# Performance work log

Hardware: AMD Instinct MI355X
Metric: run time of the kernel (lower is better)

The kernel has to match this reference:

```python
import jax, jax.numpy as jnp
import numpy as np

N_NODES = 50000
N_EDGES = 800000
HIDDEN = 128


def setup_inputs() -> dict:
    key = jax.random.key(0)
    ks = jax.random.split(key, 8)
    z = jax.random.normal(ks[0], (N_NODES, HIDDEN), dtype=jnp.float32)
    weights = jax.random.normal(ks[1], (N_EDGES, 1), dtype=jnp.float32)
    sources = jax.random.randint(ks[2], (N_EDGES,), 0, N_NODES)
    dests = jax.random.randint(ks[3], (N_EDGES,), 0, N_NODES)
    # Linear params (stored [in, out]); scale ~ 1/sqrt(fan_in) like torch default
    in_m = 2 * HIDDEN + 1
    in_u = 2 * HIDDEN
    Wm = jax.random.uniform(ks[4], (in_m, HIDDEN), dtype=jnp.float32, minval=-1.0, maxval=1.0) / np.sqrt(in_m)
    bm = jax.random.uniform(ks[5], (HIDDEN,), dtype=jnp.float32, minval=-1.0, maxval=1.0) / np.sqrt(in_m)
    Wu = jax.random.uniform(ks[6], (in_u, HIDDEN), dtype=jnp.float32, minval=-1.0, maxval=1.0) / np.sqrt(in_u)
    bu = jax.random.uniform(ks[7], (HIDDEN,), dtype=jnp.float32, minval=-1.0, maxval=1.0) / np.sqrt(in_u)
    return {"z": z, "weights": weights, "sources": sources, "dests": dests,
            "Wm": Wm, "bm": bm, "Wu": Wu, "bu": bu}


def reference(z, weights, sources, dests, Wm, bm, Wu, bu):
    n = z.shape[0]
    # gather + concat message input: [E, 2d+1]
    inp = jnp.concatenate([z[dests], z[sources], weights], axis=1)
    messages = inp @ Wm + bm                      # [E, d]
    # scatter_reduce amax over destination nodes; empty segments -> -inf
    m = jax.ops.segment_max(messages, dests, num_segments=n)
    m = jnp.where(jnp.isneginf(m), jnp.zeros_like(m), m)
    h = jnp.concatenate([z, m], axis=1) @ Wu + bu  # [N, d]
    return h
```

## Files before the change

kernel.cpp:

```cpp
#include <hip/hip_runtime.h>
#include <math.h>

#define HIDDEN 128
#define PAD_DEG 64
#define NPART 8
#define CHUNK 4096
#define CNT_STRIDE 16
#define NSCATTER_BLOCKS 256
#define XCC_GETREG_IMM 63508

typedef __attribute__((ext_vector_type(8))) _Float16 f16x8;
typedef __attribute__((ext_vector_type(4))) float f32x4;
typedef __attribute__((ext_vector_type(2))) _Float16 h2;

__device__ inline unsigned short f2h(float x) {
    _Float16 h = (_Float16)x;
    return __builtin_bit_cast(unsigned short, h);
}
__device__ inline float h2f(unsigned short u) {
    return (float)__builtin_bit_cast(_Float16, u);
}
__device__ inline float h2f_lo(unsigned int u) { return h2f((unsigned short)(u & 0xffff)); }
__device__ inline float h2f_hi(unsigned int u) { return h2f((unsigned short)(u >> 16)); }
__device__ inline h2 hmax2(h2 a, h2 b) {
    h2 r;
    r[0] = a[0] > b[0] ? a[0] : b[0];
    r[1] = a[1] > b[1] ? a[1] : b[1];
    return r;
}

__global__ void prep_kernel(const float* __restrict__ Wm, const float* __restrict__ Wu,
                            unsigned short* __restrict__ WmT0, unsigned short* __restrict__ WmT1,
                            unsigned short* __restrict__ WuT, float* __restrict__ wlast,
                            int* __restrict__ counts, int* __restrict__ tick, int n) {
    int t = blockIdx.x * blockDim.x + threadIdx.x;
    if (t < 16384) {
        int nn = t >> 7, k = t & 127;
        WmT0[t] = f2h(Wm[k * 128 + nn]);
    } else if (t < 32768) {
        int s = t - 16384;
        int nn = s >> 7, k = s & 127;
        WmT1[s] = f2h(Wm[(128 + k) * 128 + nn]);
    } else if (t < 65536) {
        int s = t - 32768;
        int nn = s >> 8, k = s & 255;
        WuT[s] = f2h(Wu[k * 128 + nn]);
    } else if (t < 65664) {
        int i = t - 65536;
        wlast[i] = Wm[256 * 128 + i];
    } else if (t < 65664 + 4 * n) {
        ((int4*)counts)[t - 65664] = make_int4(0, 0, 0, 0);
    } else if (t < 65664 + 4 * n + 128) {
        tick[t - 65664 - 4 * n] = 0;
    }
}

__global__ __launch_bounds__(256) void fused_sg(const int* __restrict__ dests,
                                                const int* __restrict__ sources,
                                                const float* __restrict__ weights,
                                                int* __restrict__ counts,
                                                int* __restrict__ tick,
                                                unsigned int* __restrict__ edge_pk,
                                                int E, int span, int n, int nchunks,
                                                const float* __restrict__ Z,
                                                const unsigned short* __restrict__ WmT0,
                                                const unsigned short* __restrict__ WmT1,
                                                unsigned short* __restrict__ P1h,
                                                unsigned short* __restrict__ P2h,
                                                int nscatter) {
    __shared__ unsigned short As[64][136];
    __shared__ unsigned short Bs[64][136];
    __shared__ int s_chunk;

    if (blockIdx.x < nscatter) {
        const int xcd = (int)(__builtin_amdgcn_s_getreg(XCC_GETREG_IMM) & 7);
        const int lo = xcd * span;
        const int hi = min(lo + span, n);

        for (int it = 0; it <= nchunks; ++it) {
            if (threadIdx.x == 0) {
                s_chunk = __hip_atomic_fetch_add(&tick[xcd * 16], 1,
                                                 __ATOMIC_RELAXED, __HIP_MEMORY_SCOPE_AGENT);
            }
            __syncthreads();
            const int chunk = s_chunk;
            __syncthreads();
            if (chunk >= nchunks || chunk < 0) break;

            const int base = chunk * CHUNK + threadIdx.x * 4;
            int dd[16];
            unsigned int pk[16];
            int pos[16];

#pragma unroll
            for (int g = 0; g < 4; ++g) {
                int e = base + g * 1024;
                if (e + 3 < E) {
                    int4 dq = *(const int4*)&dests[e];
                    int4 sq = *(const int4*)&sources[e];
                    float4 wq = *(const float4*)&weights[e];
                    dd[g * 4 + 0] = dq.x; dd[g * 4 + 1] = dq.y;
                    dd[g * 4 + 2] = dq.z; dd[g * 4 + 3] = dq.w;
                    pk[g * 4 + 0] = (unsigned int)(sq.x & 0xffff) | ((unsigned int)f2h(wq.x) << 16);
                    pk[g * 4 + 1] = (unsigned int)(sq.y & 0xffff) | ((unsigned int)f2h(wq.y) << 16);
                    pk[g * 4 + 2] = (unsigned int)(sq.z & 0xffff) | ((unsigned int)f2h(wq.z) << 16);
                    pk[g * 4 + 3] = (unsigned int)(sq.w & 0xffff) | ((unsigned int)f2h(wq.w) << 16);
                } else {
#pragma unroll
                    for (int j = 0; j < 4; ++j) {
                        int ej = e + j;
                        if (ej < E) {
                            dd[g * 4 + j] = dests[ej];
                            pk[g * 4 + j] = (unsigned int)(sources[ej] & 0xffff) |
                                            ((unsigned int)f2h(weights[ej]) << 16);
                        } else {
                            dd[g * 4 + j] = -1;
                            pk[g * 4 + j] = 0;
                        }
                    }
                }
            }

#pragma unroll
            for (int k = 0; k < 16; ++k) {
                bool act = (dd[k] >= lo) && (dd[k] < hi);
                pos[k] = act ? atomicAdd(&counts[(size_t)dd[k] * CNT_STRIDE], 1) : PAD_DEG;
            }

#pragma unroll
            for (int k = 0; k < 16; ++k) {
                if (pos[k] < PAD_DEG) {
                    edge_pk[(size_t)dd[k] * PAD_DEG + pos[k]] = pk[k];
                }
            }
        }
        return;
    }

    const int m0 = (blockIdx.x - nscatter) * 64;
    const int tid = threadIdx.x;
    const int wave = tid >> 6, lane = tid & 63;
    const int l15 = lane & 15, q = lane >> 4;
    const int wrow = wave * 16;

#pragma unroll
    for (int i = 0; i < 4; ++i) {
        int f = tid + i * 256;
        int row = f >> 4, c8 = f & 15;
        int gr = min(m0 + row, n - 1);
        const float4* src = (const float4*)&Z[(size_t)gr * 128 + c8 * 8];
        float4 a = src[0], b = src[1];
        f16x8 hv;
        hv[0] = (_Float16)a.x; hv[1] = (_Float16)a.y; hv[2] = (_Float16)a.z; hv[3] = (_Float16)a.w;
        hv[4] = (_Float16)b.x; hv[5] = (_Float16)b.y; hv[6] = (_Float16)b.z; hv[7] = (_Float16)b.w;
        *(f16x8*)&As[row][c8 * 8] = hv;
    }

    for (int part = 0; part < 2; ++part) {
        const float4* bsrc = (const float4*)(part == 0 ? WmT0 : WmT1);
        unsigned short* Out = part == 0 ? P1h : P2h;

        for (int nh = 0; nh < 2; ++nh) {
#pragma unroll
            for (int i = 0; i < 4; ++i) {
                int f = tid + i * 256;
                int row = f >> 4, c4 = f & 15;
                *(float4*)&Bs[row][c4 * 8] = bsrc[(nh * 64 + row) * 16 + c4];
            }
            __syncthreads();

            f32x4 acc[4];
#pragma unroll
            for (int nt = 0; nt < 4; ++nt) acc[nt] = (f32x4){0.f, 0.f, 0.f, 0.f};

#pragma unroll
            for (int ks = 0; ks < 4; ++ks) {
                int k0 = ks * 32;
                f16x8 a = *(const f16x8*)&As[wrow + l15][k0 + q * 8];
#pragma unroll
                for (int nt = 0; nt < 4; ++nt) {
                    f16x8 b = *(const f16x8*)&Bs[nt * 16 + l15][k0 + q * 8];
                    acc[nt] = __builtin_amdgcn_mfma_f32_16x16x32_f16(a, b, acc[nt], 0, 0, 0);
                }
            }

#pragma unroll
            for (int nt = 0; nt < 4; ++nt) {
#pragma unroll
                for (int r = 0; r < 4; ++r) {
                    int row = m0 + wrow + q * 4 + r;
                    if (row < n) Out[(size_t)row * 128 + nh * 64 + nt * 16 + l15] = f2h(acc[nt][r]);
                }
            }
            __syncthreads();
        }
    }
}

__device__ inline void ladder(const uint4* __restrict__ P2q, int pk, int cnt, int j,
                              int l16, int e4, h2 wl0, h2 wl1, h2 wl2, h2 wl3,
                              h2& a0, h2& a1, h2& a2, h2& a3) {
    for (; j + 16 <= cnt; j += 16) {
        unsigned int pa = (unsigned int)__shfl(pk, j + e4);
        unsigned int pb = (unsigned int)__shfl(pk, j + 4 + e4);
        unsigned int pc = (unsigned int)__shfl(pk, j + 8 + e4);
        unsigned int pd = (unsigned int)__shfl(pk, j + 12 + e4);
        uint4 ua = P2q[(size_t)(pa & 0xffff) * 16 + l16];
        uint4 ub = P2q[(size_t)(pb & 0xffff) * 16 + l16];
        uint4 uc = P2q[(size_t)(pc & 0xffff) * 16 + l16];
        uint4 ud = P2q[(size_t)(pd & 0xffff) * 16 + l16];
        h2 wva = __builtin_bit_cast(h2, (pa & 0xffff0000u) | (pa >> 16));
        h2 wvb = __builtin_bit_cast(h2, (pb & 0xffff0000u) | (pb >> 16));
        h2 wvc = __builtin_bit_cast(h2, (pc & 0xffff0000u) | (pc >> 16));
        h2 wvd = __builtin_bit_cast(h2, (pd & 0xffff0000u) | (pd >> 16));
        a0 = hmax2(a0, wva * wl0 + __builtin_bit_cast(h2, ua.x));
        a1 = hmax2(a1, wva * wl1 + __builtin_bit_cast(h2, ua.y));
        a2 = hmax2(a2, wva * wl2 + __builtin_bit_cast(h2, ua.z));
        a3 = hmax2(a3, wva * wl3 + __builtin_bit_cast(h2, ua.w));
        a0 = hmax2(a0, wvb * wl0 + __builtin_bit_cast(h2, ub.x));
        a1 = hmax2(a1, wvb * wl1 + __builtin_bit_cast(h2, ub.y));
        a2 = hmax2(a2, wvb * wl2 + __builtin_bit_cast(h2, ub.z));
        a3 = hmax2(a3, wvb * wl3 + __builtin_bit_cast(h2, ub.w));
        a0 = hmax2(a0, wvc * wl0 + __builtin_bit_cast(h2, uc.x));
        a1 = hmax2(a1, wvc * wl1 + __builtin_bit_cast(h2, uc.y));
        a2 = hmax2(a2, wvc * wl2 + __builtin_bit_cast(h2, uc.z));
        a3 = hmax2(a3, wvc * wl3 + __builtin_bit_cast(h2, uc.w));
        a0 = hmax2(a0, wvd * wl0 + __builtin_bit_cast(h2, ud.x));
        a1 = hmax2(a1, wvd * wl1 + __builtin_bit_cast(h2, ud.y));
        a2 = hmax2(a2, wvd * wl2 + __builtin_bit_cast(h2, ud.z));
        a3 = hmax2(a3, wvd * wl3 + __builtin_bit_cast(h2, ud.w));
    }
    for (; j + 8 <= cnt; j += 8) {
        unsigned int pa = (unsigned int)__shfl(pk, j + e4);
        unsigned int pb = (unsigned int)__shfl(pk, j + 4 + e4);
        uint4 ua = P2q[(size_t)(pa & 0xffff) * 16 + l16];
        uint4 ub = P2q[(size_t)(pb & 0xffff) * 16 + l16];
        h2 wva = __builtin_bit_cast(h2, (pa & 0xffff0000u) | (pa >> 16));
        h2 wvb = __builtin_bit_cast(h2, (pb & 0xffff0000u) | (pb >> 16));
        a0 = hmax2(a0, wva * wl0 + __builtin_bit_cast(h2, ua.x));
        a1 = hmax2(a1, wva * wl1 + __builtin_bit_cast(h2, ua.y));
        a2 = hmax2(a2, wva * wl2 + __builtin_bit_cast(h2, ua.z));
        a3 = hmax2(a3, wva * wl3 + __builtin_bit_cast(h2, ua.w));
        a0 = hmax2(a0, wvb * wl0 + __builtin_bit_cast(h2, ub.x));
        a1 = hmax2(a1, wvb * wl1 + __builtin_bit_cast(h2, ub.y));
        a2 = hmax2(a2, wvb * wl2 + __builtin_bit_cast(h2, ub.z));
        a3 = hmax2(a3, wvb * wl3 + __builtin_bit_cast(h2, ub.w));
    }
    for (; j < cnt; j += 4) {
        int idx = j + e4;
        bool valid = idx < cnt;
        unsigned int pa = (unsigned int)__shfl(pk, valid ? idx : 0);
        if (valid) {
            uint4 ua = P2q[(size_t)(pa & 0xffff) * 16 + l16];
            h2 wva = __builtin_bit_cast(h2, (pa & 0xffff0000u) | (pa >> 16));
            a0 = hmax2(a0, wva * wl0 + __builtin_bit_cast(h2, ua.x));
            a1 = hmax2(a1, wva * wl1 + __builtin_bit_cast(h2, ua.y));
            a2 = hmax2(a2, wva * wl2 + __builtin_bit_cast(h2, ua.z));
            a3 = hmax2(a3, wva * wl3 + __builtin_bit_cast(h2, ua.w));
        }
    }
}

__global__ __launch_bounds__(256) void segmax_kernel(const unsigned short* __restrict__ P1h,
                                                     const unsigned short* __restrict__ P2h,
                                                     const int* __restrict__ counts,
                                                     const unsigned int* __restrict__ edge_pk,
                                                     const float* __restrict__ wlast,
                                                     const float* __restrict__ bm,
                                                     unsigned short* __restrict__ Mh, int n) {
    const int wave = threadIdx.x >> 6;
    const int lane = threadIdx.x & 63;
    const int va = blockIdx.x * 8 + wave * 2;
    const int vb = va + 1;
    if (va >= n) return;

    const int l16 = lane & 15;
    const int e4 = lane >> 4;
    const uint4* P2q = (const uint4*)P2h;
    const int cntA = min(counts[(size_t)va * CNT_STRIDE], PAD_DEG);
    const int cntB = (vb < n) ? min(counts[(size_t)vb * CNT_STRIDE], PAD_DEG) : 0;

    int pkA = (lane < cntA) ? (int)edge_pk[(size_t)va * PAD_DEG + lane] : 0;
    int pkB = (lane < cntB) ? (int)edge_pk[(size_t)vb * PAD_DEG + lane] : 0;

    float4 wfa = ((const float4*)wlast)[l16 * 2];
    float4 wfb = ((const float4*)wlast)[l16 * 2 + 1];
    h2 wl0, wl1, wl2, wl3;
    wl0[0] = (_Float16)wfa.x; wl0[1] = (_Float16)wfa.y;
    wl1[0] = (_Float16)wfa.z; wl1[1] = (_Float16)wfa.w;
    wl2[0] = (_Float16)wfb.x; wl2[1] = (_Float16)wfb.y;
    wl3[0] = (_Float16)wfb.z; wl3[1] = (_Float16)wfb.w;

    const h2 NEGINF = __builtin_bit_cast(h2, 0xFC00FC00u);
    h2 aA0 = NEGINF, aA1 = NEGINF, aA2 = NEGINF, aA3 = NEGINF;
    h2 aB0 = NEGINF, aB1 = NEGINF, aB2 = NEGINF, aB3 = NEGINF;

    int j = 0;
    for (; j + 8 <= cntA && j + 8 <= cntB; j += 8) {
        unsigned int pa = (unsigned int)__shfl(pkA, j + e4);
        unsigned int pb = (unsigned int)__shfl(pkA, j + 4 + e4);
        unsigned int pc = (unsigned int)__shfl(pkB, j + e4);
        unsigned int pd = (unsigned int)__shfl(pkB, j + 4 + e4);
        uint4 ua = P2q[(size_t)(pa & 0xffff) * 16 + l16];
        uint4 ub = P2q[(size_t)(pb & 0xffff) * 16 + l16];
        uint4 uc = P2q[(size_t)(pc & 0xffff) * 16 + l16];
        uint4 ud = P2q[(size_t)(pd & 0xffff) * 16 + l16];
        h2 wva = __builtin_bit_cast(h2, (pa & 0xffff0000u) | (pa >> 16));
        h2 wvb = __builtin_bit_cast(h2, (pb & 0xffff0000u) | (pb >> 16));
        h2 wvc = __builtin_bit_cast(h2, (pc & 0xffff0000u) | (pc >> 16));
        h2 wvd = __builtin_bit_cast(h2, (pd & 0xffff0000u) | (pd >> 16));
        aA0 = hmax2(aA0, wva * wl0 + __builtin_bit_cast(h2, ua.x));
        aA1 = hmax2(aA1, wva * wl1 + __builtin_bit_cast(h2, ua.y));
        aA2 = hmax2(aA2, wva * wl2 + __builtin_bit_cast(h2, ua.z));
        aA3 = hmax2(aA3, wva * wl3 + __builtin_bit_cast(h2, ua.w));
        aA0 = hmax2(aA0, wvb * wl0 + __builtin_bit_cast(h2, ub.x));
        aA1 = hmax2(aA1, wvb * wl1 + __builtin_bit_cast(h2, ub.y));
        aA2 = hmax2(aA2, wvb * wl2 + __builtin_bit_cast(h2, ub.z));
        aA3 = hmax2(aA3, wvb * wl3 + __builtin_bit_cast(h2, ub.w));
        aB0 = hmax2(aB0, wvc * wl0 + __builtin_bit_cast(h2, uc.x));
        aB1 = hmax2(aB1, wvc * wl1 + __builtin_bit_cast(h2, uc.y));
        aB2 = hmax2(aB2, wvc * wl2 + __builtin_bit_cast(h2, uc.z));
        aB3 = hmax2(aB3, wvc * wl3 + __builtin_bit_cast(h2, uc.w));
        aB0 = hmax2(aB0, wvd * wl0 + __builtin_bit_cast(h2, ud.x));
        aB1 = hmax2(aB1, wvd * wl1 + __builtin_bit_cast(h2, ud.y));
        aB2 = hmax2(aB2, wvd * wl2 + __builtin_bit_cast(h2, ud.z));
        aB3 = hmax2(aB3, wvd * wl3 + __builtin_bit_cast(h2, ud.w));
    }
    ladder(P2q, pkA, cntA, j, l16, e4, wl0, wl1, wl2, wl3, aA0, aA1, aA2, aA3);
    ladder(P2q, pkB, cntB, j, l16, e4, wl0, wl1, wl2, wl3, aB0, aB1, aB2, aB3);

    aA0 = hmax2(aA0, __builtin_bit_cast(h2, __shfl_xor(__builtin_bit_cast(int, aA0), 16)));
    aA1 = hmax2(aA1, __builtin_bit_cast(h2, __shfl_xor(__builtin_bit_cast(int, aA1), 16)));
    aA2 = hmax2(aA2, __builtin_bit_cast(h2, __shfl_xor(__builtin_bit_cast(int, aA2), 16)));
    aA3 = hmax2(aA3, __builtin_bit_cast(h2, __shfl_xor(__builtin_bit_cast(int, aA3), 16)));
    aA0 = hmax2(aA0, __builtin_bit_cast(h2, __shfl_xor(__builtin_bit_cast(int, aA0), 32)));
    aA1 = hmax2(aA1, __builtin_bit_cast(h2, __shfl_xor(__builtin_bit_cast(int, aA1), 32)));
    aA2 = hmax2(aA2, __builtin_bit_cast(h2, __shfl_xor(__builtin_bit_cast(int, aA2), 32)));
    aA3 = hmax2(aA3, __builtin_bit_cast(h2, __shfl_xor(__builtin_bit_cast(int, aA3), 32)));
    aB0 = hmax2(aB0, __builtin_bit_cast(h2, __shfl_xor(__builtin_bit_cast(int, aB0), 16)));
    aB1 = hmax2(aB1, __builtin_bit_cast(h2, __shfl_xor(__builtin_bit_cast(int, aB1), 16)));
    aB2 = hmax2(aB2, __builtin_bit_cast(h2, __shfl_xor(__builtin_bit_cast(int, aB2), 16)));
    aB3 = hmax2(aB3, __builtin_bit_cast(h2, __shfl_xor(__builtin_bit_cast(int, aB3), 16)));
    aB0 = hmax2(aB0, __builtin_bit_cast(h2, __shfl_xor(__builtin_bit_cast(int, aB0), 32)));
    aB1 = hmax2(aB1, __builtin_bit_cast(h2, __shfl_xor(__builtin_bit_cast(int, aB1), 32)));
    aB2 = hmax2(aB2, __builtin_bit_cast(h2, __shfl_xor(__builtin_bit_cast(int, aB2), 32)));
    aB3 = hmax2(aB3, __builtin_bit_cast(h2, __shfl_xor(__builtin_bit_cast(int, aB3), 32)));

    if (e4 == 0) {
        float4 b0 = ((const float4*)bm)[l16 * 2];
        float4 b1 = ((const float4*)bm)[l16 * 2 + 1];
        unsigned int zh = (unsigned int)f2h(0.f);
        unsigned int zz = zh | (zh << 16);

        {
            uint4 o = make_uint4(zz, zz, zz, zz);
            if (cntA > 0) {
                uint4 p1 = ((const uint4*)P1h)[(size_t)va * 16 + l16];
                float m0 = h2f_lo(p1.x) + b0.x + (float)aA0[0];
                float m1 = h2f_hi(p1.x) + b0.y + (float)aA0[1];
                float m2 = h2f_lo(p1.y) + b0.z + (float)aA1[0];
                float m3 = h2f_hi(p1.y) + b0.w + (float)aA1[1];
                float m4 = h2f_lo(p1.z) + b1.x + (float)aA2[0];
                float m5 = h2f_hi(p1.z) + b1.y + (float)aA2[1];
                float m6 = h2f_lo(p1.w) + b1.z + (float)aA3[0];
                float m7 = h2f_hi(p1.w) + b1.w + (float)aA3[1];
                o.x = (unsigned int)f2h(m0) | ((unsigned int)f2h(m1) << 16);
                o.y = (unsigned int)f2h(m2) | ((unsigned int)f2h(m3) << 16);
                o.z = (unsigned int)f2h(m4) | ((unsigned int)f2h(m5) << 16);
                o.w = (unsigned int)f2h(m6) | ((unsigned int)f2h(m7) << 16);
            }
            ((uint4*)Mh)[(size_t)va * 16 + l16] = o;
        }
        if (vb < n) {
            uint4 o = make_uint4(zz, zz, zz, zz);
            if (cntB > 0) {
                uint4 p1 = ((const uint4*)P1h)[(size_t)vb * 16 + l16];
                float m0 = h2f_lo(p1.x) + b0.x + (float)aB0[0];
                float m1 = h2f_hi(p1.x) + b0.y + (float)aB0[1];
                float m2 = h2f_lo(p1.y) + b0.z + (float)aB1[0];
                float m3 = h2f_hi(p1.y) + b0.w + (float)aB1[1];
                float m4 = h2f_lo(p1.z) + b1.x + (float)aB2[0];
                float m5 = h2f_hi(p1.z) + b1.y + (float)aB2[1];
                float m6 = h2f_lo(p1.w) + b1.z + (float)aB3[0];
                float m7 = h2f_hi(p1.w) + b1.w + (float)aB3[1];
                o.x = (unsigned int)f2h(m0) | ((unsigned int)f2h(m1) << 16);
                o.y = (unsigned int)f2h(m2) | ((unsigned int)f2h(m3) << 16);
                o.z = (unsigned int)f2h(m4) | ((unsigned int)f2h(m5) << 16);
                o.w = (unsigned int)f2h(m6) | ((unsigned int)f2h(m7) << 16);
            }
            ((uint4*)Mh)[(size_t)vb * 16 + l16] = o;
        }
    }
}

__global__ __launch_bounds__(256) void gemm_out(const float* __restrict__ Z,
                                                const unsigned short* __restrict__ Mh,
                                                const unsigned short* __restrict__ WuT,
                                                const float* __restrict__ bu,
                                                float* __restrict__ H, int n) {
    __shared__ unsigned short As[64][136];
    __shared__ unsigned short Bs[64][136];

    const int m0 = blockIdx.x * 64;
    const int tid = threadIdx.x;
    const int wave = tid >> 6, lane = tid & 63;
    const int l15 = lane & 15, q = lane >> 4;
    const int wrow = wave * 16;

    f32x4 acc[8];
#pragma unroll
    for (int i = 0; i < 8; ++i) acc[i] = (f32x4){0.f, 0.f, 0.f, 0.f};

    for (int h = 0; h < 2; ++h) {
        if (h == 0) {
#pragma unroll
            for (int i = 0; i < 4; ++i) {
                int f = tid + i * 256;
                int row = f >> 4, c8 = f & 15;
                int gr = min(m0 + row, n - 1);
                const float4* src = (const float4*)&Z[(size_t)gr * 128 + c8 * 8];
                float4 a = src[0], b = src[1];
                f16x8 hv;
                hv[0] = (_Float16)a.x; hv[1] = (_Float16)a.y; hv[2] = (_Float16)a.z; hv[3] = (_Float16)a.w;
                hv[4] = (_Float16)b.x; hv[5] = (_Float16)b.y; hv[6] = (_Float16)b.z; hv[7] = (_Float16)b.w;
                *(f16x8*)&As[row][c8 * 8] = hv;
            }
        } else {
#pragma unroll
            for (int i = 0; i < 4; ++i) {
                int f = tid + i * 256;
                int row = f >> 4, c4 = f & 15;
                int gr = min(m0 + row, n - 1);
                *(float4*)&As[row][c4 * 8] = ((const float4*)&Mh[(size_t)gr * 128])[c4];
            }
        }

        for (int nh = 0; nh < 2; ++nh) {
#pragma unroll
            for (int i = 0; i < 4; ++i) {
                int f = tid + i * 256;
                int row = f >> 4, c4 = f & 15;
                *(float4*)&Bs[row][c4 * 8] = ((const float4*)WuT)[(nh * 64 + row) * 32 + h * 16 + c4];
            }
            __syncthreads();

#pragma unroll
            for (int ks = 0; ks < 4; ++ks) {
                int k0 = ks * 32;
                f16x8 a = *(const f16x8*)&As[wrow + l15][k0 + q * 8];
#pragma unroll
                for (int nt = 0; nt < 4; ++nt) {
                    f16x8 b = *(const f16x8*)&Bs[nt * 16 + l15][k0 + q * 8];
                    acc[nh * 4 + nt] = __builtin_amdgcn_mfma_f32_16x16x32_f16(a, b, acc[nh * 4 + nt], 0, 0, 0);
                }
            }
            __syncthreads();
        }
    }

#pragma unroll
    for (int nh = 0; nh < 2; ++nh) {
#pragma unroll
        for (int nt = 0; nt < 4; ++nt) {
            int col = nh * 64 + nt * 16 + l15;
            float bias = bu[col];
#pragma unroll
            for (int r = 0; r < 4; ++r) {
                int row = m0 + wrow + q * 4 + r;
                if (row < n) H[(size_t)row * 128 + col] = acc[nh * 4 + nt][r] + bias;
            }
        }
    }
}

extern "C" void kernel_launch(void* const* d_in, const int* in_sizes, int n_in,
                              void* d_out, int out_size, void* d_ws, size_t ws_size,
                              hipStream_t stream) {
    const float* z = (const float*)d_in[0];
    const float* weights = (const float*)d_in[1];
    const int* sources = (const int*)d_in[2];
    const int* dests = (const int*)d_in[3];
    const float* Wm = (const float*)d_in[4];
    const float* bm = (const float*)d_in[5];
    const float* Wu = (const float*)d_in[6];
    const float* bu = (const float*)d_in[7];

    const int n = in_sizes[0] / HIDDEN;
    const int E = in_sizes[1];
    float* H = (float*)d_out;

    char* w = (char*)d_ws;
    auto alloc = [&](size_t bytes) { void* p = w; w += (bytes + 255) & ~(size_t)255; return p; };
    unsigned short* P1h = (unsigned short*)alloc((size_t)n * 128 * 2);
    unsigned short* Mh  = (unsigned short*)alloc((size_t)n * 128 * 2);
    unsigned short* WmT0 = (unsigned short*)alloc(16384 * 2);
    unsigned short* WmT1 = (unsigned short*)alloc(16384 * 2);
    unsigned short* WuT  = (unsigned short*)alloc(32768 * 2);
    float* wlast = (float*)alloc(128 * 4);
    int* counts  = (int*)alloc((size_t)n * CNT_STRIDE * 4);
    int* tick    = (int*)alloc(128 * 4);
    unsigned int* edge_pk = (unsigned int*)alloc((size_t)n * PAD_DEG * 4);

    unsigned short* P2h = (unsigned short*)d_out;

    const int mblocks = (n + 63) / 64;
    const int prep_threads = 65664 + 4 * n + 128;
    const int span = (n + NPART - 1) / NPART;
    const int nchunks = (E + CHUNK - 1) / CHUNK;
    const int nscatter = NSCATTER_BLOCKS;

    prep_kernel<<<(prep_threads + 255) / 256, 256, 0, stream>>>(Wm, Wu, WmT0, WmT1, WuT,
                                                                wlast, counts, tick, n);
    fused_sg<<<nscatter + mblocks, 256, 0, stream>>>(dests, sources, weights, counts, tick,
                                                     edge_pk, E, span, n, nchunks,
                                                     z, WmT0, WmT1, P1h, P2h, nscatter);
    segmax_kernel<<<(n + 7) / 8, 256, 0, stream>>>(P1h, P2h, counts, edge_pk,
                                                   wlast, bm, Mh, n);
    gemm_out<<<mblocks, 256, 0, stream>>>(z, Mh, WuT, bu, H, n);
}
```

Before: 180.8 us.

## Split output GEMM and overlap Z-half with segment-max gather kernel

The output projection is split into a Z·Wu_top part and an M·Wu_bottom part. The Z part runs as extra blocks in the same launch as the segment-max kernel, so the dense GEMM can overlap the gather-bound aggregation. A separate kernel then adds M·Wu_bottom into H with a read-modify-write. M is written in place over the P1h buffer, and P2h moves from the output buffer into workspace so H can be written early. In exchange, H is read and written a second time, and the segmax blocks now share the GPU with GEMM blocks.

```diff
diff --git a/kernel.cpp b/kernel.cpp
--- a/kernel.cpp
+++ b/kernel.cpp
@@ -261,143 +261,208 @@
     }
 }
 
-__global__ __launch_bounds__(256) void segmax_kernel(const unsigned short* __restrict__ P1h,
-                                                     const unsigned short* __restrict__ P2h,
-                                                     const int* __restrict__ counts,
-                                                     const unsigned int* __restrict__ edge_pk,
-                                                     const float* __restrict__ wlast,
-                                                     const float* __restrict__ bm,
-                                                     unsigned short* __restrict__ Mh, int n) {
-    const int wave = threadIdx.x >> 6;
-    const int lane = threadIdx.x & 63;
-    const int va = blockIdx.x * 8 + wave * 2;
-    const int vb = va + 1;
-    if (va >= n) return;
-
-    const int l16 = lane & 15;
-    const int e4 = lane >> 4;
-    const uint4* P2q = (const uint4*)P2h;
-    const int cntA = min(counts[(size_t)va * CNT_STRIDE], PAD_DEG);
-    const int cntB = (vb < n) ? min(counts[(size_t)vb * CNT_STRIDE], PAD_DEG) : 0;
-
-    int pkA = (lane < cntA) ? (int)edge_pk[(size_t)va * PAD_DEG + lane] : 0;
-    int pkB = (lane < cntB) ? (int)edge_pk[(size_t)vb * PAD_DEG + lane] : 0;
-
-    float4 wfa = ((const float4*)wlast)[l16 * 2];
-    float4 wfb = ((const float4*)wlast)[l16 * 2 + 1];
-    h2 wl0, wl1, wl2, wl3;
-    wl0[0] = (_Float16)wfa.x; wl0[1] = (_Float16)wfa.y;
-    wl1[0] = (_Float16)wfa.z; wl1[1] = (_Float16)wfa.w;
-    wl2[0] = (_Float16)wfb.x; wl2[1] = (_Float16)wfb.y;
-    wl3[0] = (_Float16)wfb.z; wl3[1] = (_Float16)wfb.w;
-
-    const h2 NEGINF = __builtin_bit_cast(h2, 0xFC00FC00u);
-    h2 aA0 = NEGINF, aA1 = NEGINF, aA2 = NEGINF, aA3 = NEGINF;
-    h2 aB0 = NEGINF, aB1 = NEGINF, aB2 = NEGINF, aB3 = NEGINF;
-
-    int j = 0;
-    for (; j + 8 <= cntA && j + 8 <= cntB; j += 8) {
-        unsigned int pa = (unsigned int)__shfl(pkA, j + e4);
-        unsigned int pb = (unsigned int)__shfl(pkA, j + 4 + e4);
-        unsigned int pc = (unsigned int)__shfl(pkB, j + e4);
-        unsigned int pd = (unsigned int)__shfl(pkB, j + 4 + e4);
-        uint4 ua = P2q[(size_t)(pa & 0xffff) * 16 + l16];
-        uint4 ub = P2q[(size_t)(pb & 0xffff) * 16 + l16];
-        uint4 uc = P2q[(size_t)(pc & 0xffff) * 16 + l16];
-        uint4 ud = P2q[(size_t)(pd & 0xffff) * 16 + l16];
-        h2 wva = __builtin_bit_cast(h2, (pa & 0xffff0000u) | (pa >> 16));
-        h2 wvb = __builtin_bit_cast(h2, (pb & 0xffff0000u) | (pb >> 16));
-        h2 wvc = __builtin_bit_cast(h2, (pc & 0xffff0000u) | (pc >> 16));
-        h2 wvd = __builtin_bit_cast(h2, (pd & 0xffff0000u) | (pd >> 16));
-        aA0 = hmax2(aA0, wva * wl0 + __builtin_bit_cast(h2, ua.x));
-        aA1 = hmax2(aA1, wva * wl1 + __builtin_bit_cast(h2, ua.y));
-        aA2 = hmax2(aA2, wva * wl2 + __builtin_bit_cast(h2, ua.z));
-        aA3 = hmax2(aA3, wva * wl3 + __builtin_bit_cast(h2, ua.w));
-        aA0 = hmax2(aA0, wvb * wl0 + __builtin_bit_cast(h2, ub.x));
-        aA1 = hmax2(aA1, wvb * wl1 + __builtin_bit_cast(h2, ub.y));
-        aA2 = hmax2(aA2, wvb * wl2 + __builtin_bit_cast(h2, ub.z));
-        aA3 = hmax2(aA3, wvb * wl3 + __builtin_bit_cast(h2, ub.w));
-        aB0 = hmax2(aB0, wvc * wl0 + __builtin_bit_cast(h2, uc.x));
-        aB1 = hmax2(aB1, wvc * wl1 + __builtin_bit_cast(h2, uc.y));
-        aB2 = hmax2(aB2, wvc * wl2 + __builtin_bit_cast(h2, uc.z));
-        aB3 = hmax2(aB3, wvc * wl3 + __builtin_bit_cast(h2, uc.w));
-        aB0 = hmax2(aB0, wvd * wl0 + __builtin_bit_cast(h2, ud.x));
-        aB1 = hmax2(aB1, wvd * wl1 + __builtin_bit_cast(h2, ud.y));
-        aB2 = hmax2(aB2, wvd * wl2 + __builtin_bit_cast(h2, ud.z));
-        aB3 = hmax2(aB3, wvd * wl3 + __builtin_bit_cast(h2, ud.w));
-    }
-    ladder(P2q, pkA, cntA, j, l16, e4, wl0, wl1, wl2, wl3, aA0, aA1, aA2, aA3);
-    ladder(P2q, pkB, cntB, j, l16, e4, wl0, wl1, wl2, wl3, aB0, aB1, aB2, aB3);
-
-    aA0 = hmax2(aA0, __builtin_bit_cast(h2, __shfl_xor(__builtin_bit_cast(int, aA0), 16)));
-    aA1 = hmax2(aA1, __builtin_bit_cast(h2, __shfl_xor(__builtin_bit_cast(int, aA1), 16)));
-    aA2 = hmax2(aA2, __builtin_bit_cast(h2, __shfl_xor(__builtin_bit_cast(int, aA2), 16)));
-    aA3 = hmax2(aA3, __builtin_bit_cast(h2, __shfl_xor(__builtin_bit_cast(int, aA3), 16)));
-    aA0 = hmax2(aA0, __builtin_bit_cast(h2, __shfl_xor(__builtin_bit_cast(int, aA0), 32)));
-    aA1 = hmax2(aA1, __builtin_bit_cast(h2, __shfl_xor(__builtin_bit_cast(int, aA1), 32)));
-    aA2 = hmax2(aA2, __builtin_bit_cast(h2, __shfl_xor(__builtin_bit_cast(int, aA2), 32)));
-    aA3 = hmax2(aA3, __builtin_bit_cast(h2, __shfl_xor(__builtin_bit_cast(int, aA3), 32)));
-    aB0 = hmax2(aB0, __builtin_bit_cast(h2, __shfl_xor(__builtin_bit_cast(int, aB0), 16)));
-    aB1 = hmax2(aB1, __builtin_bit_cast(h2, __shfl_xor(__builtin_bit_cast(int, aB1), 16)));
-    aB2 = hmax2(aB2, __builtin_bit_cast(h2, __shfl_xor(__builtin_bit_cast(int, aB2), 16)));
-    aB3 = hmax2(aB3, __builtin_bit_cast(h2, __shfl_xor(__builtin_bit_cast(int, aB3), 16)));
-    aB0 = hmax2(aB0, __builtin_bit_cast(h2, __shfl_xor(__builtin_bit_cast(int, aB0), 32)));
-    aB1 = hmax2(aB1, __builtin_bit_cast(h2, __shfl_xor(__builtin_bit_cast(int, aB1), 32)));
-    aB2 = hmax2(aB2, __builtin_bit_cast(h2, __shfl_xor(__builtin_bit_cast(int, aB2), 32)));
-    aB3 = hmax2(aB3, __builtin_bit_cast(h2, __shfl_xor(__builtin_bit_cast(int, aB3), 32)));
-
-    if (e4 == 0) {
-        float4 b0 = ((const float4*)bm)[l16 * 2];
-        float4 b1 = ((const float4*)bm)[l16 * 2 + 1];
-        unsigned int zh = (unsigned int)f2h(0.f);
-        unsigned int zz = zh | (zh << 16);
-
-        {
-            uint4 o = make_uint4(zz, zz, zz, zz);
-            if (cntA > 0) {
-                uint4 p1 = ((const uint4*)P1h)[(size_t)va * 16 + l16];
-                float m0 = h2f_lo(p1.x) + b0.x + (float)aA0[0];
-                float m1 = h2f_hi(p1.x) + b0.y + (float)aA0[1];
-                float m2 = h2f_lo(p1.y) + b0.z + (float)aA1[0];
-                float m3 = h2f_hi(p1.y) + b0.w + (float)aA1[1];
-                float m4 = h2f_lo(p1.z) + b1.x + (float)aA2[0];
-                float m5 = h2f_hi(p1.z) + b1.y + (float)aA2[1];
-                float m6 = h2f_lo(p1.w) + b1.z + (float)aA3[0];
-                float m7 = h2f_hi(p1.w) + b1.w + (float)aA3[1];
-                o.x = (unsigned int)f2h(m0) | ((unsigned int)f2h(m1) << 16);
-                o.y = (unsigned int)f2h(m2) | ((unsigned int)f2h(m3) << 16);
-                o.z = (unsigned int)f2h(m4) | ((unsigned int)f2h(m5) << 16);
-                o.w = (unsigned int)f2h(m6) | ((unsigned int)f2h(m7) << 16);
-            }
-            ((uint4*)Mh)[(size_t)va * 16 + l16] = o;
-        }
-        if (vb < n) {
-            uint4 o = make_uint4(zz, zz, zz, zz);
-            if (cntB > 0) {
-                uint4 p1 = ((const uint4*)P1h)[(size_t)vb * 16 + l16];
-                float m0 = h2f_lo(p1.x) + b0.x + (float)aB0[0];
-                float m1 = h2f_hi(p1.x) + b0.y + (float)aB0[1];
-                float m2 = h2f_lo(p1.y) + b0.z + (float)aB1[0];
-                float m3 = h2f_hi(p1.y) + b0.w + (float)aB1[1];
-                float m4 = h2f_lo(p1.z) + b1.x + (float)aB2[0];
-                float m5 = h2f_hi(p1.z) + b1.y + (float)aB2[1];
-                float m6 = h2f_lo(p1.w) + b1.z + (float)aB3[0];
-                float m7 = h2f_hi(p1.w) + b1.w + (float)aB3[1];
-                o.x = (unsigned int)f2h(m0) | ((unsigned int)f2h(m1) << 16);
-                o.y = (unsigned int)f2h(m2) | ((unsigned int)f2h(m3) << 16);
-                o.z = (unsigned int)f2h(m4) | ((unsigned int)f2h(m5) << 16);
-                o.w = (unsigned int)f2h(m6) | ((unsigned int)f2h(m7) << 16);
-            }
-            ((uint4*)Mh)[(size_t)vb * 16 + l16] = o;
-        }
-    }
-}
-
-__global__ __launch_bounds__(256) void gemm_out(const float* __restrict__ Z,
-                                                const unsigned short* __restrict__ Mh,
-                                                const unsigned short* __restrict__ WuT,
-                                                const float* __restrict__ bu,
-                                                float* __restrict__ H, int n) {
+__global__ __launch_bounds__(256) void seg_gz(const unsigned short* P1h,
+                                              const unsigned short* __restrict__ P2h,
+                                              const int* __restrict__ counts,
+                                              const unsigned int* __restrict__ edge_pk,
+                                              const float* __restrict__ wlast,
+                                              const float* __restrict__ bm,
+                                              unsigned short* Mh,
+                                              const float* __restrict__ Z,
+                                              const unsigned short* __restrict__ WuT,
+                                              const float* __restrict__ bu,
+                                              float* __restrict__ H,
+                                              int n, int nseg) {
+    __shared__ unsigned short As[64][136];
+    __shared__ unsigned short Bs[64][136];
+
+    if (blockIdx.x < nseg) {
+        const int wave = threadIdx.x >> 6;
+        const int lane = threadIdx.x & 63;
+        const int va = blockIdx.x * 8 + wave * 2;
+        const int vb = va + 1;
+        if (va >= n) return;
+
+        const int l16 = lane & 15;
+        const int e4 = lane >> 4;
+        const uint4* P2q = (const uint4*)P2h;
+        const int cntA = min(counts[(size_t)va * CNT_STRIDE], PAD_DEG);
+        const int cntB = (vb < n) ? min(counts[(size_t)vb * CNT_STRIDE], PAD_DEG) : 0;
+
+        int pkA = (lane < cntA) ? (int)edge_pk[(size_t)va * PAD_DEG + lane] : 0;
+        int pkB = (lane < cntB) ? (int)edge_pk[(size_t)vb * PAD_DEG + lane] : 0;
+
+        float4 wfa = ((const float4*)wlast)[l16 * 2];
+        float4 wfb = ((const float4*)wlast)[l16 * 2 + 1];
+        h2 wl0, wl1, wl2, wl3;
+        wl0[0] = (_Float16)wfa.x; wl0[1] = (_Float16)wfa.y;
+        wl1[0] = (_Float16)wfa.z; wl1[1] = (_Float16)wfa.w;
+        wl2[0] = (_Float16)wfb.x; wl2[1] = (_Float16)wfb.y;
+        wl3[0] = (_Float16)wfb.z; wl3[1] = (_Float16)wfb.w;
+
+        const h2 NEGINF = __builtin_bit_cast(h2, 0xFC00FC00u);
+        h2 aA0 = NEGINF, aA1 = NEGINF, aA2 = NEGINF, aA3 = NEGINF;
+        h2 aB0 = NEGINF, aB1 = NEGINF, aB2 = NEGINF, aB3 = NEGINF;
+
+        int j = 0;
+        for (; j + 8 <= cntA && j + 8 <= cntB; j += 8) {
+            unsigned int pa = (unsigned int)__shfl(pkA, j + e4);
+            unsigned int pb = (unsigned int)__shfl(pkA, j + 4 + e4);
+            unsigned int pc = (unsigned int)__shfl(pkB, j + e4);
+            unsigned int pd = (unsigned int)__shfl(pkB, j + 4 + e4);
+            uint4 ua = P2q[(size_t)(pa & 0xffff) * 16 + l16];
+            uint4 ub = P2q[(size_t)(pb & 0xffff) * 16 + l16];
+            uint4 uc = P2q[(size_t)(pc & 0xffff) * 16 + l16];
+            uint4 ud = P2q[(size_t)(pd & 0xffff) * 16 + l16];
+            h2 wva = __builtin_bit_cast(h2, (pa & 0xffff0000u) | (pa >> 16));
+            h2 wvb = __builtin_bit_cast(h2, (pb & 0xffff0000u) | (pb >> 16));
+            h2 wvc = __builtin_bit_cast(h2, (pc & 0xffff0000u) | (pc >> 16));
+            h2 wvd = __builtin_bit_cast(h2, (pd & 0xffff0000u) | (pd >> 16));
+            aA0 = hmax2(aA0, wva * wl0 + __builtin_bit_cast(h2, ua.x));
+            aA1 = hmax2(aA1, wva * wl1 + __builtin_bit_cast(h2, ua.y));
+            aA2 = hmax2(aA2, wva * wl2 + __builtin_bit_cast(h2, ua.z));
+            aA3 = hmax2(aA3, wva * wl3 + __builtin_bit_cast(h2, ua.w));
+            aA0 = hmax2(aA0, wvb * wl0 + __builtin_bit_cast(h2, ub.x));
+            aA1 = hmax2(aA1, wvb * wl1 + __builtin_bit_cast(h2, ub.y));
+            aA2 = hmax2(aA2, wvb * wl2 + __builtin_bit_cast(h2, ub.z));
+            aA3 = hmax2(aA3, wvb * wl3 + __builtin_bit_cast(h2, ub.w));
+            aB0 = hmax2(aB0, wvc * wl0 + __builtin_bit_cast(h2, uc.x));
+            aB1 = hmax2(aB1, wvc * wl1 + __builtin_bit_cast(h2, uc.y));
+            aB2 = hmax2(aB2, wvc * wl2 + __builtin_bit_cast(h2, uc.z));
+            aB3 = hmax2(aB3, wvc * wl3 + __builtin_bit_cast(h2, uc.w));
+            aB0 = hmax2(aB0, wvd * wl0 + __builtin_bit_cast(h2, ud.x));
+            aB1 = hmax2(aB1, wvd * wl1 + __builtin_bit_cast(h2, ud.y));
+            aB2 = hmax2(aB2, wvd * wl2 + __builtin_bit_cast(h2, ud.z));
+            aB3 = hmax2(aB3, wvd * wl3 + __builtin_bit_cast(h2, ud.w));
+        }
+        ladder(P2q, pkA, cntA, j, l16, e4, wl0, wl1, wl2, wl3, aA0, aA1, aA2, aA3);
+        ladder(P2q, pkB, cntB, j, l16, e4, wl0, wl1, wl2, wl3, aB0, aB1, aB2, aB3);
+
+        aA0 = hmax2(aA0, __builtin_bit_cast(h2, __shfl_xor(__builtin_bit_cast(int, aA0), 16)));
+        aA1 = hmax2(aA1, __builtin_bit_cast(h2, __shfl_xor(__builtin_bit_cast(int, aA1), 16)));
+        aA2 = hmax2(aA2, __builtin_bit_cast(h2, __shfl_xor(__builtin_bit_cast(int, aA2), 16)));
+        aA3 = hmax2(aA3, __builtin_bit_cast(h2, __shfl_xor(__builtin_bit_cast(int, aA3), 16)));
+        aA0 = hmax2(aA0, __builtin_bit_cast(h2, __shfl_xor(__builtin_bit_cast(int, aA0), 32)));
+        aA1 = hmax2(aA1, __builtin_bit_cast(h2, __shfl_xor(__builtin_bit_cast(int, aA1), 32)));
+        aA2 = hmax2(aA2, __builtin_bit_cast(h2, __shfl_xor(__builtin_bit_cast(int, aA2), 32)));
+        aA3 = hmax2(aA3, __builtin_bit_cast(h2, __shfl_xor(__builtin_bit_cast(int, aA3), 32)));
+        aB0 = hmax2(aB0, __builtin_bit_cast(h2, __shfl_xor(__builtin_bit_cast(int, aB0), 16)));
+        aB1 = hmax2(aB1, __builtin_bit_cast(h2, __shfl_xor(__builtin_bit_cast(int, aB1), 16)));
+        aB2 = hmax2(aB2, __builtin_bit_cast(h2, __shfl_xor(__builtin_bit_cast(int, aB2), 16)));
+        aB3 = hmax2(aB3, __builtin_bit_cast(h2, __shfl_xor(__builtin_bit_cast(int, aB3), 16)));
+        aB0 = hmax2(aB0, __builtin_bit_cast(h2, __shfl_xor(__builtin_bit_cast(int, aB0), 32)));
+        aB1 = hmax2(aB1, __builtin_bit_cast(h2, __shfl_xor(__builtin_bit_cast(int, aB1), 32)));
+        aB2 = hmax2(aB2, __builtin_bit_cast(h2, __shfl_xor(__builtin_bit_cast(int, aB2), 32)));
+        aB3 = hmax2(aB3, __builtin_bit_cast(h2, __shfl_xor(__builtin_bit_cast(int, aB3), 32)));
+
+        if (e4 == 0) {
+            float4 b0 = ((const float4*)bm)[l16 * 2];
+            float4 b1 = ((const float4*)bm)[l16 * 2 + 1];
+            unsigned int zh = (unsigned int)f2h(0.f);
+            unsigned int zz = zh | (zh << 16);
+
+            {
+                uint4 o = make_uint4(zz, zz, zz, zz);
+                if (cntA > 0) {
+                    uint4 p1 = ((const uint4*)P1h)[(size_t)va * 16 + l16];
+                    float m0 = h2f_lo(p1.x) + b0.x + (float)aA0[0];
+                    float m1 = h2f_hi(p1.x) + b0.y + (float)aA0[1];
+                    float m2 = h2f_lo(p1.y) + b0.z + (float)aA1[0];
+                    float m3 = h2f_hi(p1.y) + b0.w + (float)aA1[1];
+                    float m4 = h2f_lo(p1.z) + b1.x + (float)aA2[0];
+                    float m5 = h2f_hi(p1.z) + b1.y + (float)aA2[1];
+                    float m6 = h2f_lo(p1.w) + b1.z + (float)aA3[0];
+                    float m7 = h2f_hi(p1.w) + b1.w + (float)aA3[1];
+                    o.x = (unsigned int)f2h(m0) | ((unsigned int)f2h(m1) << 16);
+                    o.y = (unsigned int)f2h(m2) | ((unsigned int)f2h(m3) << 16);
+                    o.z = (unsigned int)f2h(m4) | ((unsigned int)f2h(m5) << 16);
+                    o.w = (unsigned int)f2h(m6) | ((unsigned int)f2h(m7) << 16);
+                }
+                ((uint4*)Mh)[(size_t)va * 16 + l16] = o;
+            }
+            if (vb < n) {
+                uint4 o = make_uint4(zz, zz, zz, zz);
+                if (cntB > 0) {
+                    uint4 p1 = ((const uint4*)P1h)[(size_t)vb * 16 + l16];
+                    float m0 = h2f_lo(p1.x) + b0.x + (float)aB0[0];
+                    float m1 = h2f_hi(p1.x) + b0.y + (float)aB0[1];
+                    float m2 = h2f_lo(p1.y) + b0.z + (float)aB1[0];
+                    float m3 = h2f_hi(p1.y) + b0.w + (float)aB1[1];
+                    float m4 = h2f_lo(p1.z) + b1.x + (float)aB2[0];
+                    float m5 = h2f_hi(p1.z) + b1.y + (float)aB2[1];
+                    float m6 = h2f_lo(p1.w) + b1.z + (float)aB3[0];
+                    float m7 = h2f_hi(p1.w) + b1.w + (float)aB3[1];
+                    o.x = (unsigned int)f2h(m0) | ((unsigned int)f2h(m1) << 16);
+                    o.y = (unsigned int)f2h(m2) | ((unsigned int)f2h(m3) << 16);
+                    o.z = (unsigned int)f2h(m4) | ((unsigned int)f2h(m5) << 16);
+                    o.w = (unsigned int)f2h(m6) | ((unsigned int)f2h(m7) << 16);
+                }
+                ((uint4*)Mh)[(size_t)vb * 16 + l16] = o;
+            }
+        }
+        return;
+    }
+
+    const int m0 = (blockIdx.x - nseg) * 64;
+    const int tid = threadIdx.x;
+    const int wave = tid >> 6, lane = tid & 63;
+    const int l15 = lane & 15, q = lane >> 4;
+    const int wrow = wave * 16;
+
+#pragma unroll
+    for (int i = 0; i < 4; ++i) {
+        int f = tid + i * 256;
+        int row = f >> 4, c8 = f & 15;
+        int gr = min(m0 + row, n - 1);
+        const float4* src = (const float4*)&Z[(size_t)gr * 128 + c8 * 8];
+        float4 a = src[0], b = src[1];
+        f16x8 hv;
+        hv[0] = (_Float16)a.x; hv[1] = (_Float16)a.y; hv[2] = (_Float16)a.z; hv[3] = (_Float16)a.w;
+        hv[4] = (_Float16)b.x; hv[5] = (_Float16)b.y; hv[6] = (_Float16)b.z; hv[7] = (_Float16)b.w;
+        *(f16x8*)&As[row][c8 * 8] = hv;
+    }
+
+    for (int nh = 0; nh < 2; ++nh) {
+#pragma unroll
+        for (int i = 0; i < 4; ++i) {
+            int f = tid + i * 256;
+            int row = f >> 4, c4 = f & 15;
+            *(float4*)&Bs[row][c4 * 8] = ((const float4*)WuT)[(nh * 64 + row) * 32 + c4];
+        }
+        __syncthreads();
+
+        f32x4 acc[4];
+#pragma unroll
+        for (int nt = 0; nt < 4; ++nt) acc[nt] = (f32x4){0.f, 0.f, 0.f, 0.f};
+
+#pragma unroll
+        for (int ks = 0; ks < 4; ++ks) {
+            int k0 = ks * 32;
+            f16x8 a = *(const f16x8*)&As[wrow + l15][k0 + q * 8];
+#pragma unroll
+            for (int nt = 0; nt < 4; ++nt) {
+                f16x8 b = *(const f16x8*)&Bs[nt * 16 + l15][k0 + q * 8];
+                acc[nt] = __builtin_amdgcn_mfma_f32_16x16x32_f16(a, b, acc[nt], 0, 0, 0);
+            }
+        }
+
+#pragma unroll
+        for (int nt = 0; nt < 4; ++nt) {
+            int col = nh * 64 + nt * 16 + l15;
+            float bias = bu[col];
+#pragma unroll
+            for (int r = 0; r < 4; ++r) {
+                int row = m0 + wrow + q * 4 + r;
+                if (row < n) H[(size_t)row * 128 + col] = acc[nt][r] + bias;
+            }
+        }
+        __syncthreads();
+    }
+}
+
+__global__ __launch_bounds__(256) void gemm_m(const unsigned short* __restrict__ Mh,
+                                              const unsigned short* __restrict__ WuT,
+                                              float* __restrict__ H, int n) {
     __shared__ unsigned short As[64][136];
     __shared__ unsigned short Bs[64][136];
 
@@ -407,69 +472,48 @@
     const int l15 = lane & 15, q = lane >> 4;
     const int wrow = wave * 16;
 
-    f32x4 acc[8];
-#pragma unroll
-    for (int i = 0; i < 8; ++i) acc[i] = (f32x4){0.f, 0.f, 0.f, 0.f};
-
-    for (int h = 0; h < 2; ++h) {
-        if (h == 0) {
-#pragma unroll
-            for (int i = 0; i < 4; ++i) {
-                int f = tid + i * 256;
-                int row = f >> 4, c8 = f & 15;
-                int gr = min(m0 + row, n - 1);
-                const float4* src = (const float4*)&Z[(size_t)gr * 128 + c8 * 8];
-                float4 a = src[0], b = src[1];
-                f16x8 hv;
-                hv[0] = (_Float16)a.x; hv[1] = (_Float16)a.y; hv[2] = (_Float16)a.z; hv[3] = (_Float16)a.w;
-                hv[4] = (_Float16)b.x; hv[5] = (_Float16)b.y; hv[6] = (_Float16)b.z; hv[7] = (_Float16)b.w;
-                *(f16x8*)&As[row][c8 * 8] = hv;
-            }
-        } else {
-#pragma unroll
-            for (int i = 0; i < 4; ++i) {
-                int f = tid + i * 256;
-                int row = f >> 4, c4 = f & 15;
-                int gr = min(m0 + row, n - 1);
-                *(float4*)&As[row][c4 * 8] = ((const float4*)&Mh[(size_t)gr * 128])[c4];
-            }
-        }
-
-        for (int nh = 0; nh < 2; ++nh) {
-#pragma unroll
-            for (int i = 0; i < 4; ++i) {
-                int f = tid + i * 256;
-                int row = f >> 4, c4 = f & 15;
-                *(float4*)&Bs[row][c4 * 8] = ((const float4*)WuT)[(nh * 64 + row) * 32 + h * 16 + c4];
-            }
-            __syncthreads();
-
-#pragma unroll
-            for (int ks = 0; ks < 4; ++ks) {
-                int k0 = ks * 32;
-                f16x8 a = *(const f16x8*)&As[wrow + l15][k0 + q * 8];
-#pragma unroll
-                for (int nt = 0; nt < 4; ++nt) {
-                    f16x8 b = *(const f16x8*)&Bs[nt * 16 + l15][k0 + q * 8];
-                    acc[nh * 4 + nt] = __builtin_amdgcn_mfma_f32_16x16x32_f16(a, b, acc[nh * 4 + nt], 0, 0, 0);
-                }
-            }
-            __syncthreads();
-        }
-    }
-
-#pragma unroll
+#pragma unroll
+    for (int i = 0; i < 4; ++i) {
+        int f = tid + i * 256;
+        int row = f >> 4, c4 = f & 15;
+        int gr = min(m0 + row, n - 1);
+        *(float4*)&As[row][c4 * 8] = ((const float4*)&Mh[(size_t)gr * 128])[c4];
+    }
+
     for (int nh = 0; nh < 2; ++nh) {
+#pragma unroll
+        for (int i = 0; i < 4; ++i) {
+            int f = tid + i * 256;
+            int row = f >> 4, c4 = f & 15;
+            *(float4*)&Bs[row][c4 * 8] = ((const float4*)WuT)[(nh * 64 + row) * 32 + 16 + c4];
+        }
+        __syncthreads();
+
+        f32x4 acc[4];
+#pragma unroll
+        for (int nt = 0; nt < 4; ++nt) acc[nt] = (f32x4){0.f, 0.f, 0.f, 0.f};
+
+#pragma unroll
+        for (int ks = 0; ks < 4; ++ks) {
+            int k0 = ks * 32;
+            f16x8 a = *(const f16x8*)&As[wrow + l15][k0 + q * 8];
+#pragma unroll
+            for (int nt = 0; nt < 4; ++nt) {
+                f16x8 b = *(const f16x8*)&Bs[nt * 16 + l15][k0 + q * 8];
+                acc[nt] = __builtin_amdgcn_mfma_f32_16x16x32_f16(a, b, acc[nt], 0, 0, 0);
+            }
+        }
+
 #pragma unroll
         for (int nt = 0; nt < 4; ++nt) {
             int col = nh * 64 + nt * 16 + l15;
-            float bias = bu[col];
 #pragma unroll
             for (int r = 0; r < 4; ++r) {
                 int row = m0 + wrow + q * 4 + r;
-                if (row < n) H[(size_t)row * 128 + col] = acc[nh * 4 + nt][r] + bias;
-            }
-        }
+                if (row < n) H[(size_t)row * 128 + col] += acc[nt][r];
+            }
+        }
+        __syncthreads();
     }
 }
 
@@ -492,7 +536,7 @@
     char* w = (char*)d_ws;
     auto alloc = [&](size_t bytes) { void* p = w; w += (bytes + 255) & ~(size_t)255; return p; };
     unsigned short* P1h = (unsigned short*)alloc((size_t)n * 128 * 2);
-    unsigned short* Mh  = (unsigned short*)alloc((size_t)n * 128 * 2);
+    unsigned short* P2h = (unsigned short*)alloc((size_t)n * 128 * 2);
     unsigned short* WmT0 = (unsigned short*)alloc(16384 * 2);
     unsigned short* WmT1 = (unsigned short*)alloc(16384 * 2);
     unsigned short* WuT  = (unsigned short*)alloc(32768 * 2);
@@ -501,20 +545,19 @@
     int* tick    = (int*)alloc(128 * 4);
     unsigned int* edge_pk = (unsigned int*)alloc((size_t)n * PAD_DEG * 4);
 
-    unsigned short* P2h = (unsigned short*)d_out;
-
     const int mblocks = (n + 63) / 64;
     const int prep_threads = 65664 + 4 * n + 128;
     const int span = (n + NPART - 1) / NPART;
     const int nchunks = (E + CHUNK - 1) / CHUNK;
     const int nscatter = NSCATTER_BLOCKS;
+    const int nseg = (n + 7) / 8;
 
     prep_kernel<<<(prep_threads + 255) / 256, 256, 0, stream>>>(Wm, Wu, WmT0, WmT1, WuT,
                                                                 wlast, counts, tick, n);
     fused_sg<<<nscatter + mblocks, 256, 0, stream>>>(dests, sources, weights, counts, tick,
                                                      edge_pk, E, span, n, nchunks,
                                                      z, WmT0, WmT1, P1h, P2h, nscatter);
-    segmax_kernel<<<(n + 7) / 8, 256, 0, stream>>>(P1h, P2h, counts, edge_pk,
-                                                   wlast, bm, Mh, n);
-    gemm_out<<<mblocks, 256, 0, stream>>>(z, Mh, WuT, bu, H, n);
-}
+    seg_gz<<<nseg + mblocks, 256, 0, stream>>>(P1h, P2h, counts, edge_pk, wlast, bm,
+                                               P1h, z, WuT, bu, H, n, nseg);
+    gemm_m<<<mblocks, 256, 0, stream>>>(P1h, WuT, H, n);
+}
```

New measurement: 206.8 us. 14.4% more time.
